# Performance work log

Measured on AMD Instinct MI355X. Metric: run time of the kernel, lower is better.

The kernel has to match this reference:

```python
import jax, jax.numpy as jnp
import numpy as np

B, T, DM = 2, 2048, 2048
HQ, HKV, D = 16, 4, 128
MULT = 0.08838834764831845  # attn_output_multiplier = 1/sqrt(key_size)
ROPE_BASE = 10000.0


def rotate_half(x):
    x1, x2 = jnp.split(x, 2, axis=-1)
    return jnp.concatenate((-x2, x1), axis=-1)


def rope_tables(seq_len, dim, dtype):
    inv_freq = 1.0 / (ROPE_BASE ** (jnp.arange(0, dim, 2, dtype=jnp.float32) / dim))
    t = jnp.arange(seq_len, dtype=jnp.float32)
    freqs = jnp.outer(t, inv_freq)              # [T, D/2]
    emb = jnp.concatenate((freqs, freqs), axis=-1)  # [T, D]
    cos = jnp.cos(emb)[None, :, None, :].astype(dtype)  # [1, T, 1, D]
    sin = jnp.sin(emb)[None, :, None, :].astype(dtype)
    return cos, sin


def setup_inputs() -> dict:
    key = jax.random.key(0)
    ks = jax.random.split(key, 5)
    s = 1.0 / np.sqrt(DM)
    x = jax.random.normal(ks[0], (B, T, DM), dtype=jnp.float32)
    Wq = jax.random.normal(ks[1], (DM, HQ * D), dtype=jnp.float32) * s
    Wk = jax.random.normal(ks[2], (DM, HKV * D), dtype=jnp.float32) * s
    Wv = jax.random.normal(ks[3], (DM, HKV * D), dtype=jnp.float32) * s
    Wo = jax.random.normal(ks[4], (HQ * D, DM), dtype=jnp.float32) * s
    mask = jnp.tril(jnp.ones((T, T), dtype=bool))[None, None]  # [1,1,T,T] causal
    return {"x": x, "mask": mask, "Wq": Wq, "Wk": Wk, "Wv": Wv, "Wo": Wo}


def reference(x, mask, Wq, Wk, Wv, Wo):
    Bx, Tx, _ = x.shape
    q = (x @ Wq).reshape(Bx, Tx, HQ, D)
    k = (x @ Wk).reshape(Bx, Tx, HKV, D)
    v = (x @ Wv).reshape(Bx, Tx, HKV, D)
    cos, sin = rope_tables(Tx, D, x.dtype)
    q = q * cos + rotate_half(q) * sin
    k = k * cos + rotate_half(k) * sin
    n_rep = HQ // HKV
    k = jnp.repeat(k, n_rep, axis=2)  # [B,T,HQ,D] (repeat_interleave)
    v = jnp.repeat(v, n_rep, axis=2)
    logits = jnp.einsum('bqhd,bkhd->bhqk', q, k) * MULT
    logits = jnp.where(mask, logits, jnp.float32(-jnp.inf))
    attn = jax.nn.softmax(logits.astype(jnp.float32), axis=-1).astype(x.dtype)
    out = jnp.einsum('bhqk,bkhd->bqhd', attn, v).reshape(Bx, Tx, HQ * D)
    return out @ Wo
```

## Files before the change

### kernel.cpp

```cpp
#include <hip/hip_runtime.h>
#include <cstdint>
#include <cstddef>

#define T_SEQ 2048
#define DMODEL 2048
#define HQ 16
#define HKV 4
#define HD 128

typedef __attribute__((ext_vector_type(4))) float f32x4;
typedef __attribute__((ext_vector_type(8))) short bf16x8;
typedef __attribute__((ext_vector_type(4))) short short4v;
typedef __attribute__((ext_vector_type(2))) short short2v;
typedef __attribute__((ext_vector_type(4))) unsigned uint4v;

__device__ __forceinline__ short f2bf(float f) {
  unsigned u = __builtin_bit_cast(unsigned, f);
  u = (u + 0x7FFFu + ((u >> 16) & 1u)) >> 16;
  return (short)u;
}
__device__ __forceinline__ float bf2f(short s) {
  unsigned u = ((unsigned)(unsigned short)s) << 16;
  return __builtin_bit_cast(float, u);
}
__device__ __forceinline__ unsigned pk_hi16(float a, float b) {
  return __builtin_amdgcn_perm(__builtin_bit_cast(unsigned, b),
                               __builtin_bit_cast(unsigned, a), 0x07060302u);
}

__device__ __forceinline__ void g2lds16(const void* g, void* l) {
  __builtin_amdgcn_global_load_lds(
      (const __attribute__((address_space(1))) void*)g,
      (__attribute__((address_space(3))) void*)l, 16, 0, 0);
}

__global__ void cvt_kernel(const float* __restrict__ src, short* __restrict__ dst, int n) {
  int idx = blockIdx.x * 256 + threadIdx.x;
  int i = idx * 4;
  if (i >= n) return;
  float4 v = *(const float4*)(src + i);
  short4v o;
  o[0] = f2bf(v.x); o[1] = f2bf(v.y); o[2] = f2bf(v.z); o[3] = f2bf(v.w);
  *(short4v*)(dst + i) = o;
}

__global__ void transpose_cvt4(const float* __restrict__ s0, const float* __restrict__ s1,
                               const float* __restrict__ s2, const float* __restrict__ s3,
                               short* __restrict__ d0, short* __restrict__ d1,
                               short* __restrict__ d2, short* __restrict__ d3) {
  __shared__ float tile[32][33];
  const int z = blockIdx.z;
  const float* src = (z == 0) ? s0 : (z == 1) ? s1 : (z == 2) ? s2 : s3;
  short* dst = (z == 0) ? d0 : (z == 1) ? d1 : (z == 2) ? d2 : d3;
  const int C = (z == 1 || z == 2) ? 512 : 2048;
  const int R = 2048;
  int c0 = blockIdx.x * 32, r0 = blockIdx.y * 32;
  if (c0 >= C) return;
  int tx = threadIdx.x, ty = threadIdx.y;
  #pragma unroll
  for (int i = 0; i < 32; i += 8)
    tile[ty + i][tx] = src[(size_t)(r0 + ty + i) * C + c0 + tx];
  __syncthreads();
  #pragma unroll
  for (int i = 0; i < 32; i += 8)
    dst[(size_t)(c0 + ty + i) * R + r0 + tx] = f2bf(tile[tx][ty + i]);
}

template <int MODE>
__global__ __launch_bounds__(256, 2) void gemm_kernel(
    const short* __restrict__ A, const short* __restrict__ BT,
    void* __restrict__ C0, void* __restrict__ C1, void* __restrict__ C2,
    int M, int N, int K)
{
  __shared__ short As[128 * 64];
  __shared__ short Bs[128 * 64];
  const int tid = threadIdx.x;
  const int lane = tid & 63, w = tid >> 6;
  const int l15 = lane & 15, g = lane >> 4;
  const int m0 = blockIdx.y * 128, n0 = blockIdx.x * 128;
  const int wm = (w >> 1) * 64, wn = (w & 1) * 64;

  const int srow = tid >> 3;
  const int sc   = tid & 7;

  f32x4 acc[4][4] = {};

  for (int k0 = 0; k0 < K; k0 += 64) {
    __syncthreads();
    #pragma unroll
    for (int call = 0; call < 4; call++) {
      int row = call * 32 + srow;
      int csw = sc ^ (row & 7);
      g2lds16(A + (size_t)(m0 + row) * K + k0 + csw * 8,
              (char*)As + call * 4096 + w * 1024);
      g2lds16(BT + (size_t)(n0 + row) * K + k0 + csw * 8,
              (char*)Bs + call * 4096 + w * 1024);
    }
    __syncthreads();
    #pragma unroll
    for (int kk = 0; kk < 2; kk++) {
      bf16x8 af[4], bfr[4];
      #pragma unroll
      for (int mi = 0; mi < 4; mi++) {
        int row = wm + mi * 16 + l15;
        int ch = (kk * 4 + g) ^ (row & 7);
        af[mi] = *(const bf16x8*)(As + row * 64 + ch * 8);
      }
      #pragma unroll
      for (int ni = 0; ni < 4; ni++) {
        int row = wn + ni * 16 + l15;
        int ch = (kk * 4 + g) ^ (row & 7);
        bfr[ni] = *(const bf16x8*)(Bs + row * 64 + ch * 8);
      }
      #pragma unroll
      for (int mi = 0; mi < 4; mi++)
        #pragma unroll
        for (int ni = 0; ni < 4; ni++)
          acc[mi][ni] = __builtin_amdgcn_mfma_f32_16x16x32_bf16(af[mi], bfr[ni], acc[mi][ni], 0, 0, 0);
    }
  }

  if (MODE == 1) {
    float* C = (float*)C0;
    #pragma unroll
    for (int mi = 0; mi < 4; mi++)
      #pragma unroll
      for (int r = 0; r < 4; r++) {
        int m = m0 + wm + mi * 16 + g * 4 + r;
        #pragma unroll
        for (int ni = 0; ni < 4; ni++)
          C[(size_t)m * N + n0 + wn + ni * 16 + l15] = acc[mi][ni][r];
      }
  } else {
    short* Cb; int ldc, nc;
    if (n0 < 2048)      { Cb = (short*)C0; ldc = 2048; nc = n0; }
    else if (n0 < 2560) { Cb = (short*)C1; ldc = 512;  nc = n0 - 2048; }
    else                { Cb = (short*)C2; ldc = 512;  nc = n0 - 2560; }
    #pragma unroll
    for (int mi = 0; mi < 4; mi++)
      #pragma unroll
      for (int r = 0; r < 4; r++) {
        int m = m0 + wm + mi * 16 + g * 4 + r;
        #pragma unroll
        for (int ni = 0; ni < 4; ni++)
          Cb[(size_t)m * ldc + nc + wn + ni * 16 + l15] = f2bf(acc[mi][ni][r]);
      }
  }
}

__global__ void rope_all(short* __restrict__ qbuf, short* __restrict__ kbuf, float qscale) {
  int idx = blockIdx.x * 256 + threadIdx.x;
  short* buf; int NH; float scale;
  if (idx < 4194304) { buf = qbuf; NH = HQ; scale = qscale; }
  else               { buf = kbuf; NH = HKV; scale = 1.0f; idx -= 4194304; }
  int i = idx & 63;
  int th = idx >> 6;
  int t = (th / NH) % T_SEQ;
  size_t base = (size_t)th * 128;
  float invf = exp2f(-(float)i * 0.20762050593046014f);
  float theta = (float)t * invf;
  float sn, cs;
  sincosf(theta, &sn, &cs);
  float a = bf2f(buf[base + i]);
  float b = bf2f(buf[base + 64 + i]);
  buf[base + i]      = f2bf((a * cs - b * sn) * scale);
  buf[base + 64 + i] = f2bf((b * cs + a * sn) * scale);
}

__global__ __launch_bounds__(512, 4) void attn_kernel(
    const short* __restrict__ qg, const short* __restrict__ kg,
    const short* __restrict__ vg, short* __restrict__ og)
{
  __shared__ short Ks[2][64 * 128];
  __shared__ short Vt[128 * 64];
  const int tid = threadIdx.x;
  const int lane = tid & 63, w = tid >> 6;
  const int l15 = lane & 15, g = lane >> 4;
  const int b = blockIdx.z;
  const int qti = b ? (15 - (int)blockIdx.x) : (int)blockIdx.x;
  const int qt0 = qti * 128;
  const int h = blockIdx.y, hk = h >> 2;
  const int qw0 = qt0 + w * 16;

  bf16x8 qf[4];
  {
    size_t t = (size_t)b * T_SEQ + qw0 + l15;
    const short* qp = qg + (t * HQ + h) * HD;
    #pragma unroll
    for (int ks = 0; ks < 4; ks++)
      qf[ks] = *(const bf16x8*)(qp + ks * 32 + g * 8);
  }

  f32x4 of[8] = {};
  float m2 = -INFINITY;
  float ls = 0.f;

  const short* kbase = kg + ((size_t)b * T_SEQ * HKV + hk) * HD;
  const short* vbase = vg + ((size_t)b * T_SEQ * HKV + hk) * HD;

  const int kv2 = (tid & 31) * 2;
  const int d8s = (tid >> 5) * 8;
  const int p0 = (kv2 >> 5) * 32 + ((kv2 & 15) >> 2) * 8 + ((kv2 >> 4) & 1) * 4 + (kv2 & 3);
  const int nt = (qt0 + 128) >> 6;

  bf16x8 vr[2];

  auto stageK = [&](int t, int nb) {
    #pragma unroll
    for (int call = 0; call < 2; call++) {
      int tau = call * 512 + tid;
      int kv = tau >> 4, c = tau & 15;
      g2lds16(kbase + (size_t)(t * 64 + kv) * (HKV * HD) + ((c ^ (kv & 7)) << 3),
              (char*)Ks[nb] + call * 8192 + w * 1024);
    }
  };
  auto loadV = [&](int t) {
    const short* vp = vbase + (size_t)(t * 64 + kv2) * (HKV * HD) + d8s;
    vr[0] = *(const bf16x8*)(vp);
    vr[1] = *(const bf16x8*)(vp + HKV * HD);
  };
  auto writeV = [&]() {
    #pragma unroll
    for (int e = 0; e < 8; e++) {
      int row = d8s + e;
      int addr = row * 64 + (((p0 >> 3) ^ e) << 3) + (p0 & 7);
      short2v t2; t2[0] = vr[0][e]; t2[1] = vr[1][e];
      *(short2v*)(&Vt[addr]) = t2;
    }
  };

  stageK(0, 0);
  loadV(0);
  __syncthreads();
  writeV();
  __syncthreads();

  int cur = 0;
  for (int t = 0; t < nt; t++) {
    const int kv0 = t * 64;
    const bool haveNext = (t + 1 < nt);
    if (haveNext) { loadV(t + 1); stageK(t + 1, cur ^ 1); }

    if (kv0 <= qw0 + 15) {
      const short* Kc = Ks[cur];
      f32x4 sacc[4] = {};
      __builtin_amdgcn_s_setprio(1);
      #pragma unroll
      for (int ks = 0; ks < 4; ks++) {
        bf16x8 kf[4];
        #pragma unroll
        for (int kt = 0; kt < 4; kt++) {
          int row = kt * 16 + l15;
          int ch = (ks * 4 + g) ^ (row & 7);
          kf[kt] = *(const bf16x8*)(Kc + row * 128 + ch * 8);
        }
        #pragma unroll
        for (int kt = 0; kt < 4; kt++)
          sacc[kt] = __builtin_amdgcn_mfma_f32_16x16x32_bf16(kf[kt], qf[ks], sacc[kt], 0, 0, 0);
      }
      __builtin_amdgcn_s_setprio(0);
      const bool needmask = (kv0 + 63) > qw0;
      const int qpos = qw0 + l15;
      float vmax = -INFINITY;
      #pragma unroll
      for (int kt = 0; kt < 4; kt++)
        #pragma unroll
        for (int r = 0; r < 4; r++) {
          int kvpos = kv0 + kt * 16 + g * 4 + r;
          float sv = sacc[kt][r];
          if (needmask && kvpos > qpos) sv = -INFINITY;
          sacc[kt][r] = sv;
          vmax = fmaxf(vmax, sv);
        }
      vmax = fmaxf(vmax, __shfl_xor(vmax, 16));
      vmax = fmaxf(vmax, __shfl_xor(vmax, 32));
      if (!__all(vmax <= m2 + 8.0f)) {
        float mnew = fmaxf(m2, vmax);
        float resc = exp2f(m2 - mnew);
        m2 = mnew;
        ls *= resc;
        #pragma unroll
        for (int dc = 0; dc < 8; dc++) of[dc] *= resc;
      }
      float lsum = 0.f;
      #pragma unroll
      for (int kt = 0; kt < 4; kt++)
        #pragma unroll
        for (int r = 0; r < 4; r++) {
          float p = exp2f(sacc[kt][r] - m2);
          sacc[kt][r] = p;
          lsum += p;
        }
      lsum += __shfl_xor(lsum, 16);
      lsum += __shfl_xor(lsum, 32);
      ls += lsum;
      bf16x8 pb[2];
      #pragma unroll
      for (int ktw = 0; ktw < 2; ktw++) {
        uint4v pw;
        pw[0] = pk_hi16(sacc[2 * ktw][0], sacc[2 * ktw][1]);
        pw[1] = pk_hi16(sacc[2 * ktw][2], sacc[2 * ktw][3]);
        pw[2] = pk_hi16(sacc[2 * ktw + 1][0], sacc[2 * ktw + 1][1]);
        pw[3] = pk_hi16(sacc[2 * ktw + 1][2], sacc[2 * ktw + 1][3]);
        pb[ktw] = __builtin_bit_cast(bf16x8, pw);
      }
      __builtin_amdgcn_s_setprio(1);
      #pragma unroll
      for (int ktw = 0; ktw < 2; ktw++)
        #pragma unroll
        for (int dc = 0; dc < 8; dc++) {
          int row = dc * 16 + l15;
          bf16x8 vf = *(const bf16x8*)(&Vt[row * 64 + ((ktw * 32 + g * 8) ^ ((l15 & 7) << 3))]);
          of[dc] = __builtin_amdgcn_mfma_f32_16x16x32_bf16(vf, pb[ktw], of[dc], 0, 0, 0);
        }
      __builtin_amdgcn_s_setprio(0);
    }

    __syncthreads();
    if (haveNext) writeV();
    __syncthreads();
    cur ^= 1;
  }

  {
    float inv = 1.0f / ls;
    size_t t = (size_t)b * T_SEQ + qw0 + l15;
    short* op = og + (t * HQ + h) * HD;
    #pragma unroll
    for (int dc = 0; dc < 8; dc++) {
      short4v o;
      #pragma unroll
      for (int r = 0; r < 4; r++) o[r] = f2bf(of[dc][r] * inv);
      *(short4v*)(op + dc * 16 + g * 4) = o;
    }
  }
}

extern "C" void kernel_launch(void* const* d_in, const int* in_sizes, int n_in,
                              void* d_out, int out_size, void* d_ws, size_t ws_size,
                              hipStream_t stream) {
  (void)in_sizes; (void)n_in; (void)out_size; (void)ws_size;
  const float* x  = (const float*)d_in[0];
  const float* Wq = (const float*)d_in[2];
  const float* Wk = (const float*)d_in[3];
  const float* Wv = (const float*)d_in[4];
  const float* Wo = (const float*)d_in[5];

  char* ws = (char*)d_ws;
  short* xb   = (short*)(ws);
  short* wall = (short*)(ws + 16777216);
  short* wkT  = wall + (size_t)2048 * 2048;
  short* wvT  = wall + (size_t)2560 * 2048;
  short* woT  = (short*)(ws + 29360128);
  short* qb   = (short*)(ws + 37748736);
  short* kb   = (short*)(ws + 54525952);
  short* vb   = (short*)(ws + 58720256);
  short* ab   = (short*)(ws + 62914560);

  const float MULT = 0.08838834764831845f;
  const float LOG2E = 1.4426950408889634f;
  const float QSCALE = MULT * LOG2E;

  dim3 tb(32, 8);
  cvt_kernel<<<8192, 256, 0, stream>>>(x, xb, 8388608);
  transpose_cvt4<<<dim3(64, 64, 4), tb, 0, stream>>>(Wq, Wk, Wv, Wo, wall, wkT, wvT, woT);

  gemm_kernel<2><<<dim3(24, 32), 256, 0, stream>>>(xb, wall, qb, kb, vb, 4096, 3072, 2048);

  rope_all<<<20480, 256, 0, stream>>>(qb, kb, QSCALE);

  attn_kernel<<<dim3(16, 16, 2), 512, 0, stream>>>(qb, kb, vb, ab);

  gemm_kernel<1><<<dim3(16, 32), 256, 0, stream>>>(ab, woT, d_out, nullptr, nullptr, 4096, 2048, 2048);
}
```

Before: 206.4 us.

## Share K/V tiles across GQA head group with two q-chunks per wave

The attention block now covers one KV head and all four query heads that share it, over a 64-row query tile. Each wave handles 32 query rows (two 16-row chunks) of one query head. Every K/V tile loaded into LDS is therefore reused by four query heads instead of one, cutting K/V global traffic and staging per unit of work, and each wave issues twice the MFMAs per K fragment load. The cost is more registers (launch bounds drop to 2 blocks/CU), fewer blocks in the grid (256 vs 512), and the row-sum reduction is deferred to the end.

```diff
diff --git a/kernel.cpp b/kernel.cpp
--- a/kernel.cpp
+++ b/kernel.cpp
@@ -167,7 +167,7 @@
   buf[base + 64 + i] = f2bf((b * cs + a * sn) * scale);
 }
 
-__global__ __launch_bounds__(512, 4) void attn_kernel(
+__global__ __launch_bounds__(512, 2) void attn_kernel(
     const short* __restrict__ qg, const short* __restrict__ kg,
     const short* __restrict__ vg, short* __restrict__ og)
 {
@@ -177,23 +177,25 @@
   const int lane = tid & 63, w = tid >> 6;
   const int l15 = lane & 15, g = lane >> 4;
   const int b = blockIdx.z;
-  const int qti = b ? (15 - (int)blockIdx.x) : (int)blockIdx.x;
-  const int qt0 = qti * 128;
-  const int h = blockIdx.y, hk = h >> 2;
-  const int qw0 = qt0 + w * 16;
-
-  bf16x8 qf[4];
-  {
-    size_t t = (size_t)b * T_SEQ + qw0 + l15;
+  const int qh = b ? (31 - (int)blockIdx.x) : (int)blockIdx.x;
+  const int qb0 = qh * 64;
+  const int hk = blockIdx.y;
+  const int h = hk * 4 + (w & 3);
+  const int qw0 = qb0 + (w >> 2) * 32;
+
+  bf16x8 qf[2][4];
+  #pragma unroll
+  for (int qc = 0; qc < 2; qc++) {
+    size_t t = (size_t)b * T_SEQ + qw0 + qc * 16 + l15;
     const short* qp = qg + (t * HQ + h) * HD;
     #pragma unroll
     for (int ks = 0; ks < 4; ks++)
-      qf[ks] = *(const bf16x8*)(qp + ks * 32 + g * 8);
-  }
-
-  f32x4 of[8] = {};
-  float m2 = -INFINITY;
-  float ls = 0.f;
+      qf[qc][ks] = *(const bf16x8*)(qp + ks * 32 + g * 8);
+  }
+
+  f32x4 of[2][8] = {};
+  float m2[2] = {-INFINITY, -INFINITY};
+  float ls[2] = {0.f, 0.f};
 
   const short* kbase = kg + ((size_t)b * T_SEQ * HKV + hk) * HD;
   const short* vbase = vg + ((size_t)b * T_SEQ * HKV + hk) * HD;
@@ -201,7 +203,7 @@
   const int kv2 = (tid & 31) * 2;
   const int d8s = (tid >> 5) * 8;
   const int p0 = (kv2 >> 5) * 32 + ((kv2 & 15) >> 2) * 8 + ((kv2 >> 4) & 1) * 4 + (kv2 & 3);
-  const int nt = (qt0 + 128) >> 6;
+  const int nt = qh + 1;
 
   bf16x8 vr[2];
 
@@ -241,9 +243,9 @@
     const bool haveNext = (t + 1 < nt);
     if (haveNext) { loadV(t + 1); stageK(t + 1, cur ^ 1); }
 
-    if (kv0 <= qw0 + 15) {
+    if (kv0 <= qw0 + 31) {
       const short* Kc = Ks[cur];
-      f32x4 sacc[4] = {};
+      f32x4 sacc[4][2] = {};
       __builtin_amdgcn_s_setprio(1);
       #pragma unroll
       for (int ks = 0; ks < 4; ks++) {
@@ -256,53 +258,55 @@
         }
         #pragma unroll
         for (int kt = 0; kt < 4; kt++)
-          sacc[kt] = __builtin_amdgcn_mfma_f32_16x16x32_bf16(kf[kt], qf[ks], sacc[kt], 0, 0, 0);
+          #pragma unroll
+          for (int qc = 0; qc < 2; qc++)
+            sacc[kt][qc] = __builtin_amdgcn_mfma_f32_16x16x32_bf16(kf[kt], qf[qc][ks], sacc[kt][qc], 0, 0, 0);
       }
       __builtin_amdgcn_s_setprio(0);
       const bool needmask = (kv0 + 63) > qw0;
-      const int qpos = qw0 + l15;
-      float vmax = -INFINITY;
-      #pragma unroll
-      for (int kt = 0; kt < 4; kt++)
-        #pragma unroll
-        for (int r = 0; r < 4; r++) {
-          int kvpos = kv0 + kt * 16 + g * 4 + r;
-          float sv = sacc[kt][r];
-          if (needmask && kvpos > qpos) sv = -INFINITY;
-          sacc[kt][r] = sv;
-          vmax = fmaxf(vmax, sv);
+      bf16x8 pb[2][2];
+      #pragma unroll
+      for (int qc = 0; qc < 2; qc++) {
+        int qpos = qw0 + qc * 16 + l15;
+        float vmax = -INFINITY;
+        #pragma unroll
+        for (int kt = 0; kt < 4; kt++)
+          #pragma unroll
+          for (int r = 0; r < 4; r++) {
+            int kvpos = kv0 + kt * 16 + g * 4 + r;
+            float sv = sacc[kt][qc][r];
+            if (needmask && kvpos > qpos) sv = -INFINITY;
+            sacc[kt][qc][r] = sv;
+            vmax = fmaxf(vmax, sv);
+          }
+        vmax = fmaxf(vmax, __shfl_xor(vmax, 16));
+        vmax = fmaxf(vmax, __shfl_xor(vmax, 32));
+        if (!__all(vmax <= m2[qc] + 8.0f)) {
+          float mnew = fmaxf(m2[qc], vmax);
+          float resc = exp2f(m2[qc] - mnew);
+          m2[qc] = mnew;
+          ls[qc] *= resc;
+          #pragma unroll
+          for (int dc = 0; dc < 8; dc++) of[qc][dc] *= resc;
         }
-      vmax = fmaxf(vmax, __shfl_xor(vmax, 16));
-      vmax = fmaxf(vmax, __shfl_xor(vmax, 32));
-      if (!__all(vmax <= m2 + 8.0f)) {
-        float mnew = fmaxf(m2, vmax);
-        float resc = exp2f(m2 - mnew);
-        m2 = mnew;
-        ls *= resc;
-        #pragma unroll
-        for (int dc = 0; dc < 8; dc++) of[dc] *= resc;
-      }
-      float lsum = 0.f;
-      #pragma unroll
-      for (int kt = 0; kt < 4; kt++)
-        #pragma unroll
-        for (int r = 0; r < 4; r++) {
-          float p = exp2f(sacc[kt][r] - m2);
-          sacc[kt][r] = p;
-          lsum += p;
+        float mref = m2[qc];
+        #pragma unroll
+        for (int kt = 0; kt < 4; kt++)
+          #pragma unroll
+          for (int r = 0; r < 4; r++) {
+            float p = exp2f(sacc[kt][qc][r] - mref);
+            sacc[kt][qc][r] = p;
+            ls[qc] += p;
+          }
+        #pragma unroll
+        for (int ktw = 0; ktw < 2; ktw++) {
+          uint4v pw;
+          pw[0] = pk_hi16(sacc[2 * ktw][qc][0], sacc[2 * ktw][qc][1]);
+          pw[1] = pk_hi16(sacc[2 * ktw][qc][2], sacc[2 * ktw][qc][3]);
+          pw[2] = pk_hi16(sacc[2 * ktw + 1][qc][0], sacc[2 * ktw + 1][qc][1]);
+          pw[3] = pk_hi16(sacc[2 * ktw + 1][qc][2], sacc[2 * ktw + 1][qc][3]);
+          pb[ktw][qc] = __builtin_bit_cast(bf16x8, pw);
         }
-      lsum += __shfl_xor(lsum, 16);
-      lsum += __shfl_xor(lsum, 32);
-      ls += lsum;
-      bf16x8 pb[2];
-      #pragma unroll
-      for (int ktw = 0; ktw < 2; ktw++) {
-        uint4v pw;
-        pw[0] = pk_hi16(sacc[2 * ktw][0], sacc[2 * ktw][1]);
-        pw[1] = pk_hi16(sacc[2 * ktw][2], sacc[2 * ktw][3]);
-        pw[2] = pk_hi16(sacc[2 * ktw + 1][0], sacc[2 * ktw + 1][1]);
-        pw[3] = pk_hi16(sacc[2 * ktw + 1][2], sacc[2 * ktw + 1][3]);
-        pb[ktw] = __builtin_bit_cast(bf16x8, pw);
       }
       __builtin_amdgcn_s_setprio(1);
       #pragma unroll
@@ -311,7 +315,9 @@
         for (int dc = 0; dc < 8; dc++) {
           int row = dc * 16 + l15;
           bf16x8 vf = *(const bf16x8*)(&Vt[row * 64 + ((ktw * 32 + g * 8) ^ ((l15 & 7) << 3))]);
-          of[dc] = __builtin_amdgcn_mfma_f32_16x16x32_bf16(vf, pb[ktw], of[dc], 0, 0, 0);
+          #pragma unroll
+          for (int qc = 0; qc < 2; qc++)
+            of[qc][dc] = __builtin_amdgcn_mfma_f32_16x16x32_bf16(vf, pb[ktw][qc], of[qc][dc], 0, 0, 0);
         }
       __builtin_amdgcn_s_setprio(0);
     }
@@ -322,15 +328,19 @@
     cur ^= 1;
   }
 
-  {
-    float inv = 1.0f / ls;
-    size_t t = (size_t)b * T_SEQ + qw0 + l15;
+  #pragma unroll
+  for (int qc = 0; qc < 2; qc++) {
+    float lss = ls[qc];
+    lss += __shfl_xor(lss, 16);
+    lss += __shfl_xor(lss, 32);
+    float inv = 1.0f / lss;
+    size_t t = (size_t)b * T_SEQ + qw0 + qc * 16 + l15;
     short* op = og + (t * HQ + h) * HD;
     #pragma unroll
     for (int dc = 0; dc < 8; dc++) {
       short4v o;
       #pragma unroll
-      for (int r = 0; r < 4; r++) o[r] = f2bf(of[dc][r] * inv);
+      for (int r = 0; r < 4; r++) o[r] = f2bf(of[qc][dc][r] * inv);
       *(short4v*)(op + dc * 16 + g * 4) = o;
     }
   }
@@ -369,7 +379,7 @@
 
   rope_all<<<20480, 256, 0, stream>>>(qb, kb, QSCALE);
 
-  attn_kernel<<<dim3(16, 16, 2), 512, 0, stream>>>(qb, kb, vb, ab);
+  attn_kernel<<<dim3(32, 4, 2), 512, 0, stream>>>(qb, kb, vb, ab);
 
   gemm_kernel<1><<<dim3(16, 32), 256, 0, stream>>>(ab, woT, d_out, nullptr, nullptr, 4096, 2048, 2048);
 }
```

Result: slower. 241.3 us (+16.9%).
